# Kernel tuning notes

Measured on AMD Instinct MI355X. Metric: run time of the kernel, lower is better.

Reference implementation:

```python
import jax, jax.numpy as jnp
import numpy as np

B, S, C, H = 2, 2048, 1024, 16
D = C // H  # head dim = 64


def setup_inputs() -> dict:
    key = jax.random.key(0)
    ks = jax.random.split(key, 11)
    scale = 1.0 / np.sqrt(C)
    inp = {
        "q": jax.random.normal(ks[0], (B, S, C), dtype=jnp.float32),
        "k": jax.random.normal(ks[1], (B, S, C), dtype=jnp.float32),
        "v": jax.random.normal(ks[2], (B, S, C), dtype=jnp.float32),
        "wq": jax.random.normal(ks[3], (C, C), dtype=jnp.float32) * scale,
        "bq": jnp.zeros((C,), dtype=jnp.float32),
        "wk": jax.random.normal(ks[4], (C, C), dtype=jnp.float32) * scale,
        "bk": jnp.zeros((C,), dtype=jnp.float32),
        "wv": jax.random.normal(ks[5], (C, C), dtype=jnp.float32) * scale,
        "bv": jnp.zeros((C,), dtype=jnp.float32),
        "wo": jax.random.normal(ks[6], (C, C), dtype=jnp.float32) * scale,
        "bo": jnp.zeros((C,), dtype=jnp.float32),
    }
    return inp


def _split_heads(x):
    # [B,S,C] -> [B,H,S,D]
    b, s, _ = x.shape
    return x.reshape(b, s, H, D).transpose(0, 2, 1, 3)


def reference(q, k, v, wq, bq, wk, bk, wv, bv, wo, bo):
    qh = _split_heads(q @ wq + bq)
    kh = _split_heads(k @ wk + bk)
    vh = _split_heads(v @ wv + bv)
    scale = 1.0 / jnp.sqrt(jnp.asarray(D, dtype=qh.dtype))
    scores = jnp.einsum("bhqd,bhkd->bhqk", qh, kh) * scale  # [B,H,S,S]
    attn = jax.nn.softmax(scores, axis=-1)
    out = jnp.einsum("bhqk,bhkd->bhqd", attn, vh)  # [B,H,S,D]
    out = out.transpose(0, 2, 1, 3).reshape(q.shape[0], -1, C)  # [B,S,C]
    out = out @ wo + bo
    return out, attn
```

## Files before the change

kernel.cpp:

```cpp
#include <hip/hip_runtime.h>


#define S_  2048
#define C_  1024
#define H_  16
#define D_  64
#define BS_ 4096
#define BH_ 32

typedef unsigned short ushort_t;
typedef __attribute__((ext_vector_type(8))) short short8;
typedef __attribute__((ext_vector_type(4))) float floatx4;

#define GLDS16(gp, lp) __builtin_amdgcn_global_load_lds( \
    (__attribute__((address_space(1))) void*)(gp), \
    (__attribute__((address_space(3))) void*)(lp), 16, 0, 0)

#define MFMA16(a, b, c) __builtin_amdgcn_mfma_f32_16x16x32_bf16((a), (b), (c), 0, 0, 0)

__device__ __forceinline__ ushort_t f2bf(float x) {
  union { float f; unsigned u; } v; v.f = x;
  unsigned r = v.u + 0x7fffu + ((v.u >> 16) & 1u);
  return (ushort_t)(r >> 16);
}
__device__ __forceinline__ float bf2f(ushort_t h) {
  union { unsigned u; float f; } v; v.u = ((unsigned)h) << 16; return v.f;
}

__global__ __launch_bounds__(256) void split_plain(
    const float* __restrict__ in, ushort_t* __restrict__ hi, ushort_t* __restrict__ lo)
{
  const int i = blockIdx.x * 256 + threadIdx.x;
  float4 v = ((const float4*)in)[i];
  ushort4 h, l;
  h.x = f2bf(v.x); l.x = f2bf(v.x - bf2f(h.x));
  h.y = f2bf(v.y); l.y = f2bf(v.y - bf2f(h.y));
  h.z = f2bf(v.z); l.z = f2bf(v.z - bf2f(h.z));
  h.w = f2bf(v.w); l.w = f2bf(v.w - bf2f(h.w));
  ((ushort4*)hi)[i] = h;
  ((ushort4*)lo)[i] = l;
}

__global__ __launch_bounds__(256) void split_T(
    const float* __restrict__ W, ushort_t* __restrict__ THi, ushort_t* __restrict__ TLo)
{
  __shared__ float t[64][65];
  const int k0 = blockIdx.x * 64, n0 = blockIdx.y * 64;
  const int tid = threadIdx.x;
  const int r = tid >> 4, c4 = (tid & 15) * 4;
#pragma unroll
  for (int p = 0; p < 4; ++p) {
    float4 v = *(const float4*)&W[(size_t)(k0 + p * 16 + r) * C_ + n0 + c4];
    t[p * 16 + r][c4 + 0] = v.x;
    t[p * 16 + r][c4 + 1] = v.y;
    t[p * 16 + r][c4 + 2] = v.z;
    t[p * 16 + r][c4 + 3] = v.w;
  }
  __syncthreads();
  const int n = tid >> 2, kc = (tid & 3) * 16;
#pragma unroll
  for (int j = 0; j < 16; ++j) {
    float x = t[kc + j][n];
    ushort_t h = f2bf(x);
    const size_t idx = (size_t)(n0 + n) * C_ + k0 + kc + j;
    THi[idx] = h;
    TLo[idx] = f2bf(x - bf2f(h));
  }
}

__global__ __launch_bounds__(256) void gemm_proj(
    const ushort_t* __restrict__ Ahi, const ushort_t* __restrict__ Alo,
    const ushort_t* __restrict__ Bhi, const ushort_t* __restrict__ Blo,
    const float* __restrict__ bias,
    ushort_t* __restrict__ OHi, ushort_t* __restrict__ OLo,
    float* __restrict__ OF, int mode)
{
  __shared__ ushort_t sA[2][128 * 32];
  __shared__ ushort_t sB[2][64 * 32];

  const int tid = threadIdx.x;
  const int wv = tid >> 6, ln = tid & 63;
  const int lq = ln >> 4, lr = ln & 15;
  const int wr = wv >> 1, wc = wv & 1;
  const int r0 = blockIdx.x * 128, c0 = blockIdx.y * 64;

  const int sar = wv * 32 + (ln >> 2);
  const int sbr = wv * 16 + (ln >> 2);
  const int skc = (ln & 3) * 8;

  floatx4 acc[4][2];
#pragma unroll
  for (int m = 0; m < 4; ++m)
#pragma unroll
    for (int n = 0; n < 2; ++n) acc[m][n] = (floatx4){0.f, 0.f, 0.f, 0.f};

  for (int kt = 0; kt < 1024; kt += 32) {
    __syncthreads();
#pragma unroll
    for (int c = 0; c < 2; ++c) {
      const int row = sar + c * 16;
      GLDS16(&Ahi[(size_t)(r0 + row) * 1024 + kt + skc], &sA[0][(wv * 32 + c * 16) * 32]);
      GLDS16(&Alo[(size_t)(r0 + row) * 1024 + kt + skc], &sA[1][(wv * 32 + c * 16) * 32]);
    }
    GLDS16(&Bhi[(size_t)(c0 + sbr) * 1024 + kt + skc], &sB[0][(wv * 16) * 32]);
    GLDS16(&Blo[(size_t)(c0 + sbr) * 1024 + kt + skc], &sB[1][(wv * 16) * 32]);
    __syncthreads();

    short8 af[4][2], bf[2][2];
#pragma unroll
    for (int t = 0; t < 4; ++t) {
      af[t][0] = *(const short8*)&sA[0][(wr * 64 + t * 16 + lr) * 32 + lq * 8];
      af[t][1] = *(const short8*)&sA[1][(wr * 64 + t * 16 + lr) * 32 + lq * 8];
    }
#pragma unroll
    for (int t = 0; t < 2; ++t) {
      bf[t][0] = *(const short8*)&sB[0][(wc * 32 + t * 16 + lr) * 32 + lq * 8];
      bf[t][1] = *(const short8*)&sB[1][(wc * 32 + t * 16 + lr) * 32 + lq * 8];
    }
#pragma unroll
    for (int m = 0; m < 4; ++m)
#pragma unroll
      for (int n = 0; n < 2; ++n) {
        acc[m][n] = MFMA16(af[m][1], bf[n][0], acc[m][n]);
        acc[m][n] = MFMA16(af[m][0], bf[n][1], acc[m][n]);
        acc[m][n] = MFMA16(af[m][0], bf[n][0], acc[m][n]);
      }
  }

#pragma unroll
  for (int m = 0; m < 4; ++m) {
    const int grb = r0 + wr * 64 + m * 16 + lq * 4;
#pragma unroll
    for (int n = 0; n < 2; ++n) {
      const int gc = c0 + wc * 32 + n * 16 + lr;
      const float bs = bias[gc];
      if (mode == 2) {
#pragma unroll
        for (int r = 0; r < 4; ++r)
          OF[(size_t)(grb + r) * C_ + gc] = acc[m][n][r] + bs;
      } else if (mode == 0) {
        const int h = gc >> 6, d = gc & 63;
#pragma unroll
        for (int r = 0; r < 4; ++r) {
          const int gr = grb + r;
          const int b = gr >> 11, s = gr & (S_ - 1);
          const size_t idx = ((size_t)(b * H_ + h) * S_ + s) * D_ + d;
          float x = acc[m][n][r] + bs;
          ushort_t hx = f2bf(x);
          OHi[idx] = hx;
          OLo[idx] = f2bf(x - bf2f(hx));
        }
      } else {
        const int h = gc >> 6, d = gc & 63;
        const int b = grb >> 11, s = grb & (S_ - 1);
        const size_t idx = ((size_t)(b * H_ + h) * D_ + d) * S_ + s;
        ushort4 hv, lv;
        float x0 = acc[m][n][0] + bs, x1 = acc[m][n][1] + bs;
        float x2 = acc[m][n][2] + bs, x3 = acc[m][n][3] + bs;
        hv.x = f2bf(x0); lv.x = f2bf(x0 - bf2f(hv.x));
        hv.y = f2bf(x1); lv.y = f2bf(x1 - bf2f(hv.y));
        hv.z = f2bf(x2); lv.z = f2bf(x2 - bf2f(hv.z));
        hv.w = f2bf(x3); lv.w = f2bf(x3 - bf2f(hv.w));
        *(ushort4*)&OHi[idx] = hv;
        *(ushort4*)&OLo[idx] = lv;
      }
    }
  }
}

__global__ __launch_bounds__(256) void scores_exp(
    const ushort_t* __restrict__ QHi, const ushort_t* __restrict__ QLo,
    const ushort_t* __restrict__ KHi, const ushort_t* __restrict__ KLo,
    float* __restrict__ E, float* __restrict__ rowsum)
{
  __shared__ ushort_t sA[2][128 * 32];
  __shared__ ushort_t sB[2][128 * 32];

  const int tid = threadIdx.x;
  const int wv = tid >> 6, ln = tid & 63;
  const int lq = ln >> 4, lr = ln & 15;
  const int wr = wv >> 1, wc = wv & 1;
  const int bh = blockIdx.z;
  const int i0 = blockIdx.x * 128, j0 = blockIdx.y * 128;

  const ushort_t* Qh = QHi + (size_t)bh * S_ * D_;
  const ushort_t* Ql = QLo + (size_t)bh * S_ * D_;
  const ushort_t* Kh = KHi + (size_t)bh * S_ * D_;
  const ushort_t* Kl = KLo + (size_t)bh * S_ * D_;

  const int sar = wv * 32 + (ln >> 2);
  const int skc = (ln & 3) * 8;

  floatx4 acc[4][4];
#pragma unroll
  for (int m = 0; m < 4; ++m)
#pragma unroll
    for (int n = 0; n < 4; ++n) acc[m][n] = (floatx4){0.f, 0.f, 0.f, 0.f};

#pragma unroll
  for (int kt = 0; kt < 64; kt += 32) {
    __syncthreads();
#pragma unroll
    for (int c = 0; c < 2; ++c) {
      const int row = sar + c * 16;
      GLDS16(&Qh[(size_t)(i0 + row) * D_ + kt + skc], &sA[0][(wv * 32 + c * 16) * 32]);
      GLDS16(&Ql[(size_t)(i0 + row) * D_ + kt + skc], &sA[1][(wv * 32 + c * 16) * 32]);
      GLDS16(&Kh[(size_t)(j0 + row) * D_ + kt + skc], &sB[0][(wv * 32 + c * 16) * 32]);
      GLDS16(&Kl[(size_t)(j0 + row) * D_ + kt + skc], &sB[1][(wv * 32 + c * 16) * 32]);
    }
    __syncthreads();

    short8 af[4][2], bf[4][2];
#pragma unroll
    for (int t = 0; t < 4; ++t) {
      af[t][0] = *(const short8*)&sA[0][(wr * 64 + t * 16 + lr) * 32 + lq * 8];
      af[t][1] = *(const short8*)&sA[1][(wr * 64 + t * 16 + lr) * 32 + lq * 8];
      bf[t][0] = *(const short8*)&sB[0][(wc * 64 + t * 16 + lr) * 32 + lq * 8];
      bf[t][1] = *(const short8*)&sB[1][(wc * 64 + t * 16 + lr) * 32 + lq * 8];
    }
#pragma unroll
    for (int m = 0; m < 4; ++m)
#pragma unroll
      for (int n = 0; n < 4; ++n) {
        acc[m][n] = MFMA16(af[m][1], bf[n][0], acc[m][n]);
        acc[m][n] = MFMA16(af[m][0], bf[n][1], acc[m][n]);
        acc[m][n] = MFMA16(af[m][0], bf[n][0], acc[m][n]);
      }
  }

  float* Eb = E + (size_t)bh * S_ * S_;
  const float cexp = 0.18033688011112042f;
#pragma unroll
  for (int m = 0; m < 4; ++m) {
    const int grb = i0 + wr * 64 + m * 16 + lq * 4;
    float ps[4] = {0.f, 0.f, 0.f, 0.f};
#pragma unroll
    for (int n = 0; n < 4; ++n) {
      const int gc = j0 + wc * 64 + n * 16 + lr;
#pragma unroll
      for (int r = 0; r < 4; ++r) {
        float e = exp2f(acc[m][n][r] * cexp);
        Eb[(size_t)(grb + r) * S_ + gc] = e;
        ps[r] += e;
      }
    }
#pragma unroll
    for (int r = 0; r < 4; ++r) {
      float s = ps[r];
      s += __shfl_xor(s, 1);
      s += __shfl_xor(s, 2);
      s += __shfl_xor(s, 4);
      s += __shfl_xor(s, 8);
      if (lr == 0) atomicAdd(&rowsum[bh * S_ + grb + r], s);
    }
  }
}

__global__ __launch_bounds__(256) void pv_attn(
    float* __restrict__ E,
    const ushort_t* __restrict__ VHi, const ushort_t* __restrict__ VLo,
    const float* __restrict__ rowsum,
    ushort_t* __restrict__ OHi, ushort_t* __restrict__ OLo)
{
  __shared__ ushort_t sA[2][128 * 32];
  __shared__ ushort_t sB[2][64 * 32];

  const int tid = threadIdx.x;
  const int wv = tid >> 6, ln = tid & 63;
  const int lq = ln >> 4, lr = ln & 15;
  const int bh = blockIdx.z, b = bh >> 4, h = bh & (H_ - 1);
  const int i0 = blockIdx.x * 128;

  float* Eb = E + (size_t)bh * S_ * S_;
  const ushort_t* Vh = VHi + (size_t)bh * D_ * S_;
  const ushort_t* Vl = VLo + (size_t)bh * D_ * S_;

  const int ar = tid >> 3;
  const int ac = (tid & 7) * 4;
  float rinv_s[4];
#pragma unroll
  for (int u = 0; u < 4; ++u)
    rinv_s[u] = 1.0f / rowsum[bh * S_ + i0 + u * 32 + ar];

  const int sbr = wv * 16 + (ln >> 2);
  const int skc = (ln & 3) * 8;

  floatx4 acc[2][4];
#pragma unroll
  for (int m = 0; m < 2; ++m)
#pragma unroll
    for (int n = 0; n < 4; ++n) acc[m][n] = (floatx4){0.f, 0.f, 0.f, 0.f};

  for (int kt = 0; kt < S_; kt += 32) {
    __syncthreads();
    GLDS16(&Vh[(size_t)sbr * S_ + kt + skc], &sB[0][(wv * 16) * 32]);
    GLDS16(&Vl[(size_t)sbr * S_ + kt + skc], &sB[1][(wv * 16) * 32]);
#pragma unroll
    for (int u = 0; u < 4; ++u) {
      const int row = u * 32 + ar;
      float4 ev = *(const float4*)&Eb[(size_t)(i0 + row) * S_ + kt + ac];
      float4 nv;
      nv.x = ev.x * rinv_s[u]; nv.y = ev.y * rinv_s[u];
      nv.z = ev.z * rinv_s[u]; nv.w = ev.w * rinv_s[u];
      *(float4*)&Eb[(size_t)(i0 + row) * S_ + kt + ac] = nv;
      ushort4 h4, l4;
      h4.x = f2bf(ev.x); l4.x = f2bf(ev.x - bf2f(h4.x));
      h4.y = f2bf(ev.y); l4.y = f2bf(ev.y - bf2f(h4.y));
      h4.z = f2bf(ev.z); l4.z = f2bf(ev.z - bf2f(h4.z));
      h4.w = f2bf(ev.w); l4.w = f2bf(ev.w - bf2f(h4.w));
      *(ushort4*)&sA[0][row * 32 + ac] = h4;
      *(ushort4*)&sA[1][row * 32 + ac] = l4;
    }
    __syncthreads();

    short8 af[2][2], bf[4][2];
#pragma unroll
    for (int t = 0; t < 2; ++t) {
      af[t][0] = *(const short8*)&sA[0][(wv * 32 + t * 16 + lr) * 32 + lq * 8];
      af[t][1] = *(const short8*)&sA[1][(wv * 32 + t * 16 + lr) * 32 + lq * 8];
    }
#pragma unroll
    for (int t = 0; t < 4; ++t) {
      bf[t][0] = *(const short8*)&sB[0][(t * 16 + lr) * 32 + lq * 8];
      bf[t][1] = *(const short8*)&sB[1][(t * 16 + lr) * 32 + lq * 8];
    }
#pragma unroll
    for (int m = 0; m < 2; ++m)
#pragma unroll
      for (int n = 0; n < 4; ++n) {
        acc[m][n] = MFMA16(af[m][1], bf[n][0], acc[m][n]);
        acc[m][n] = MFMA16(af[m][0], bf[n][1], acc[m][n]);
        acc[m][n] = MFMA16(af[m][0], bf[n][0], acc[m][n]);
      }
  }

#pragma unroll
  for (int m = 0; m < 2; ++m) {
    const int rowb = wv * 32 + m * 16 + lq * 4;
#pragma unroll
    for (int r = 0; r < 4; ++r) {
      const float rv = 1.0f / rowsum[bh * S_ + i0 + rowb + r];
      const size_t orow = (size_t)(b * S_ + i0 + rowb + r) * C_ + h * D_;
#pragma unroll
      for (int n = 0; n < 4; ++n) {
        float x = acc[m][n][r] * rv;
        ushort_t hx = f2bf(x);
        OHi[orow + n * 16 + lr] = hx;
        OLo[orow + n * 16 + lr] = f2bf(x - bf2f(hx));
      }
    }
  }
}

extern "C" void kernel_launch(void* const* d_in, const int* in_sizes, int n_in,
                              void* d_out, int out_size, void* d_ws, size_t ws_size,
                              hipStream_t stream)
{
  (void)in_sizes; (void)n_in; (void)out_size; (void)ws_size;

  const float* q  = (const float*)d_in[0];
  const float* k  = (const float*)d_in[1];
  const float* v  = (const float*)d_in[2];
  const float* wq = (const float*)d_in[3];
  const float* bq = (const float*)d_in[4];
  const float* wk = (const float*)d_in[5];
  const float* bk = (const float*)d_in[6];
  const float* wv = (const float*)d_in[7];
  const float* bv = (const float*)d_in[8];
  const float* wo = (const float*)d_in[9];
  const float* bo = (const float*)d_in[10];

  const size_t NE = (size_t)BS_ * C_;

  float* outF = (float*)d_out;
  float* Ebuf = outF + NE;
  ushort_t* XSHi = (ushort_t*)d_out;
  ushort_t* XSLo = XSHi + NE;

  ushort_t* ws16 = (ushort_t*)d_ws;
  ushort_t* QhHi = ws16;           ushort_t* QhLo = QhHi + NE;
  ushort_t* KhHi = QhLo + NE;      ushort_t* KhLo = KhHi + NE;
  ushort_t* VtHi = KhLo + NE;      ushort_t* VtLo = VtHi + NE;
  ushort_t* WtHi = VtLo + NE;      ushort_t* WtLo = WtHi + (size_t)C_ * C_;
  float* rowsum = (float*)(WtLo + (size_t)C_ * C_);

  const dim3 gS(NE / 4 / 256);
  const dim3 gT(16, 16);
  const dim3 gP(BS_ / 128, C_ / 64);
  const dim3 gSc(S_ / 128, S_ / 128, BH_);
  const dim3 gPv(S_ / 128, 1, BH_);

  split_T<<<gT, 256, 0, stream>>>(wq, WtHi, WtLo);
  split_plain<<<gS, 256, 0, stream>>>(q, XSHi, XSLo);
  gemm_proj<<<gP, 256, 0, stream>>>(XSHi, XSLo, WtHi, WtLo, bq, QhHi, QhLo, nullptr, 0);
  split_T<<<gT, 256, 0, stream>>>(wk, WtHi, WtLo);
  split_plain<<<gS, 256, 0, stream>>>(k, XSHi, XSLo);
  gemm_proj<<<gP, 256, 0, stream>>>(XSHi, XSLo, WtHi, WtLo, bk, KhHi, KhLo, nullptr, 0);
  split_T<<<gT, 256, 0, stream>>>(wv, WtHi, WtLo);
  split_plain<<<gS, 256, 0, stream>>>(v, XSHi, XSLo);
  gemm_proj<<<gP, 256, 0, stream>>>(XSHi, XSLo, WtHi, WtLo, bv, VtHi, VtLo, nullptr, 1);

  hipMemsetAsync(rowsum, 0, (size_t)BH_ * S_ * sizeof(float), stream);
  scores_exp<<<gSc, 256, 0, stream>>>(QhHi, QhLo, KhHi, KhLo, Ebuf, rowsum);

  pv_attn<<<gPv, 256, 0, stream>>>(Ebuf, VtHi, VtLo, rowsum, QhHi, QhLo);

  split_T<<<gT, 256, 0, stream>>>(wo, WtHi, WtLo);
  gemm_proj<<<gP, 256, 0, stream>>>(QhHi, QhLo, WtHi, WtLo, bo, nullptr, nullptr, outF, 2);
}
```

Baseline: 1.191 ms.

## Fuse attention into flash-style PV kernel and recompute normalized probabilities for output

```diff
diff --git a/kernel.cpp b/kernel.cpp
--- a/kernel.cpp
+++ b/kernel.cpp
@@ -168,20 +168,209 @@
   }
 }
 
-__global__ __launch_bounds__(256) void scores_exp(
+__global__ __launch_bounds__(256) void attn_pv(
     const ushort_t* __restrict__ QHi, const ushort_t* __restrict__ QLo,
     const ushort_t* __restrict__ KHi, const ushort_t* __restrict__ KLo,
-    float* __restrict__ E, float* __restrict__ rowsum)
-{
-  __shared__ ushort_t sA[2][128 * 32];
-  __shared__ ushort_t sB[2][128 * 32];
+    const ushort_t* __restrict__ VHi, const ushort_t* __restrict__ VLo,
+    float* __restrict__ rowsum,
+    ushort_t* __restrict__ OHi, ushort_t* __restrict__ OLo)
+{
+  __shared__ ushort_t sQE[2][2][128 * 32];
+  __shared__ ushort_t sK[2][2][64 * 32];
+  __shared__ ushort_t sV[2][2][64 * 32];
 
   const int tid = threadIdx.x;
   const int wv = tid >> 6, ln = tid & 63;
   const int lq = ln >> 4, lr = ln & 15;
   const int wr = wv >> 1, wc = wv & 1;
-  const int bh = blockIdx.z;
-  const int i0 = blockIdx.x * 128, j0 = blockIdx.y * 128;
+
+  const int wgid = blockIdx.x;
+  const int sw = (wgid & 7) * 64 + (wgid >> 3);
+  const int bh = sw >> 4;
+  const int i0 = (sw & 15) * 128;
+  const int b = bh >> 4, h = bh & (H_ - 1);
+
+  const ushort_t* Qh = QHi + (size_t)bh * S_ * D_;
+  const ushort_t* Ql = QLo + (size_t)bh * S_ * D_;
+  const ushort_t* Kh = KHi + (size_t)bh * S_ * D_;
+  const ushort_t* Kl = KLo + (size_t)bh * S_ * D_;
+  const ushort_t* Vh = VHi + (size_t)bh * D_ * S_;
+  const ushort_t* Vl = VLo + (size_t)bh * D_ * S_;
+
+  const int srow = ln >> 2;
+  const int skc = (ln & 3) * 8;
+
+#pragma unroll
+  for (int pl = 0; pl < 2; ++pl) {
+    const ushort_t* src = pl ? Ql : Qh;
+#pragma unroll
+    for (int kp = 0; kp < 2; ++kp)
+#pragma unroll
+      for (int c = 0; c < 2; ++c)
+        GLDS16(&src[(size_t)(i0 + wv * 32 + c * 16 + srow) * D_ + kp * 32 + skc],
+               &sQE[pl][kp][(wv * 32 + c * 16) * 32]);
+  }
+  __syncthreads();
+  short8 aq[4][2][2];
+#pragma unroll
+  for (int m = 0; m < 4; ++m)
+#pragma unroll
+    for (int kp = 0; kp < 2; ++kp)
+#pragma unroll
+      for (int pl = 0; pl < 2; ++pl)
+        aq[m][kp][pl] = *(const short8*)&sQE[pl][kp][(wr * 64 + m * 16 + lr) * 32 + lq * 8];
+
+  const float cexp = 0.18033688011112042f;
+  floatx4 acc_o[4][2];
+  float ps[4][4];
+#pragma unroll
+  for (int m = 0; m < 4; ++m) {
+#pragma unroll
+    for (int n = 0; n < 2; ++n) acc_o[m][n] = (floatx4){0.f, 0.f, 0.f, 0.f};
+#pragma unroll
+    for (int r = 0; r < 4; ++r) ps[m][r] = 0.f;
+  }
+
+  for (int jt = 0; jt < 32; ++jt) {
+    const int j0 = jt * 64;
+    __syncthreads();
+#pragma unroll
+    for (int pl = 0; pl < 2; ++pl) {
+      const ushort_t* ks = pl ? Kl : Kh;
+      const ushort_t* vs = pl ? Vl : Vh;
+#pragma unroll
+      for (int kp = 0; kp < 2; ++kp)
+        GLDS16(&ks[(size_t)(j0 + wv * 16 + srow) * D_ + kp * 32 + skc],
+               &sK[pl][kp][(wv * 16) * 32]);
+#pragma unroll
+      for (int jp = 0; jp < 2; ++jp)
+        GLDS16(&vs[(size_t)(wv * 16 + srow) * S_ + j0 + jp * 32 + skc],
+               &sV[pl][jp][(wv * 16) * 32]);
+    }
+    __syncthreads();
+
+    floatx4 acc_s[4][2];
+#pragma unroll
+    for (int m = 0; m < 4; ++m)
+#pragma unroll
+      for (int n = 0; n < 2; ++n) acc_s[m][n] = (floatx4){0.f, 0.f, 0.f, 0.f};
+#pragma unroll
+    for (int kp = 0; kp < 2; ++kp) {
+      short8 bk[2][2];
+#pragma unroll
+      for (int n = 0; n < 2; ++n)
+#pragma unroll
+        for (int pl = 0; pl < 2; ++pl)
+          bk[n][pl] = *(const short8*)&sK[pl][kp][(wc * 32 + n * 16 + lr) * 32 + lq * 8];
+#pragma unroll
+      for (int m = 0; m < 4; ++m)
+#pragma unroll
+        for (int n = 0; n < 2; ++n) {
+          acc_s[m][n] = MFMA16(aq[m][kp][1], bk[n][0], acc_s[m][n]);
+          acc_s[m][n] = MFMA16(aq[m][kp][0], bk[n][1], acc_s[m][n]);
+          acc_s[m][n] = MFMA16(aq[m][kp][0], bk[n][0], acc_s[m][n]);
+        }
+    }
+
+#pragma unroll
+    for (int m = 0; m < 4; ++m)
+#pragma unroll
+      for (int n = 0; n < 2; ++n)
+#pragma unroll
+        for (int r = 0; r < 4; ++r) {
+          float e = exp2f(acc_s[m][n][r] * cexp);
+          ps[m][r] += e;
+          ushort_t eh = f2bf(e);
+          ushort_t el = f2bf(e - bf2f(eh));
+          const int row = wr * 64 + m * 16 + lq * 4 + r;
+          sQE[0][wc][row * 32 + n * 16 + lr] = eh;
+          sQE[1][wc][row * 32 + n * 16 + lr] = el;
+        }
+    __syncthreads();
+
+#pragma unroll
+    for (int kp = 0; kp < 2; ++kp) {
+      short8 ae[4][2], bv[2][2];
+#pragma unroll
+      for (int m = 0; m < 4; ++m)
+#pragma unroll
+        for (int pl = 0; pl < 2; ++pl)
+          ae[m][pl] = *(const short8*)&sQE[pl][kp][(wr * 64 + m * 16 + lr) * 32 + lq * 8];
+#pragma unroll
+      for (int n = 0; n < 2; ++n)
+#pragma unroll
+        for (int pl = 0; pl < 2; ++pl)
+          bv[n][pl] = *(const short8*)&sV[pl][kp][(wc * 32 + n * 16 + lr) * 32 + lq * 8];
+#pragma unroll
+      for (int m = 0; m < 4; ++m)
+#pragma unroll
+        for (int n = 0; n < 2; ++n) {
+          acc_o[m][n] = MFMA16(ae[m][1], bv[n][0], acc_o[m][n]);
+          acc_o[m][n] = MFMA16(ae[m][0], bv[n][1], acc_o[m][n]);
+          acc_o[m][n] = MFMA16(ae[m][0], bv[n][0], acc_o[m][n]);
+        }
+    }
+  }
+
+  __syncthreads();
+  float* sRsp = (float*)&sV[0][0][0];
+  float* sTot = sRsp + 256;
+#pragma unroll
+  for (int m = 0; m < 4; ++m)
+#pragma unroll
+    for (int r = 0; r < 4; ++r) {
+      float s = ps[m][r];
+      s += __shfl_xor(s, 1);
+      s += __shfl_xor(s, 2);
+      s += __shfl_xor(s, 4);
+      s += __shfl_xor(s, 8);
+      if (lr == 0) sRsp[wc * 128 + wr * 64 + m * 16 + lq * 4 + r] = s;
+    }
+  __syncthreads();
+  if (tid < 128) {
+    float t = sRsp[tid] + sRsp[128 + tid];
+    sTot[tid] = t;
+    rowsum[bh * S_ + i0 + tid] = t;
+  }
+  __syncthreads();
+
+#pragma unroll
+  for (int m = 0; m < 4; ++m) {
+    const int rows = wr * 64 + m * 16 + lq * 4;
+#pragma unroll
+    for (int r = 0; r < 4; ++r) {
+      const float rv = 1.0f / sTot[rows + r];
+      const size_t orow = (size_t)(b * S_ + i0 + rows + r) * C_ + h * D_;
+#pragma unroll
+      for (int n = 0; n < 2; ++n) {
+        const int d = wc * 32 + n * 16 + lr;
+        float x = acc_o[m][n][r] * rv;
+        ushort_t hx = f2bf(x);
+        OHi[orow + d] = hx;
+        OLo[orow + d] = f2bf(x - bf2f(hx));
+      }
+    }
+  }
+}
+
+__global__ __launch_bounds__(256) void attn_write(
+    const ushort_t* __restrict__ QHi, const ushort_t* __restrict__ QLo,
+    const ushort_t* __restrict__ KHi, const ushort_t* __restrict__ KLo,
+    const float* __restrict__ rowsum, float* __restrict__ attn)
+{
+  __shared__ ushort_t sA[2][128 * 32];
+  __shared__ ushort_t sB[2][128 * 32];
+
+  const int tid = threadIdx.x;
+  const int wv = tid >> 6, ln = tid & 63;
+  const int lq = ln >> 4, lr = ln & 15;
+  const int wr = wv >> 1, wc = wv & 1;
+
+  const int wgid = blockIdx.x;
+  const int sw = (wgid & 7) * 1024 + (wgid >> 3);
+  const int bh = sw >> 8;
+  const int t8 = sw & 255;
+  const int i0 = (t8 >> 4) * 128, j0 = (t8 & 15) * 128;
 
   const ushort_t* Qh = QHi + (size_t)bh * S_ * D_;
   const ushort_t* Ql = QLo + (size_t)bh * S_ * D_;
@@ -228,128 +417,31 @@
       }
   }
 
-  float* Eb = E + (size_t)bh * S_ * S_;
+  float* Eb = attn + (size_t)bh * S_ * S_;
   const float cexp = 0.18033688011112042f;
 #pragma unroll
   for (int m = 0; m < 4; ++m) {
     const int grb = i0 + wr * 64 + m * 16 + lq * 4;
-    float ps[4] = {0.f, 0.f, 0.f, 0.f};
+    float rv[4];
+#pragma unroll
+    for (int r = 0; r < 4; ++r) rv[r] = 1.0f / rowsum[bh * S_ + grb + r];
 #pragma unroll
     for (int n = 0; n < 4; ++n) {
       const int gc = j0 + wc * 64 + n * 16 + lr;
 #pragma unroll
       for (int r = 0; r < 4; ++r) {
-        float e = exp2f(acc[m][n][r] * cexp);
-        Eb[(size_t)(grb + r) * S_ + gc] = e;
-        ps[r] += e;
+        float e = exp2f(acc[m][n][r] * cexp) * rv[r];
+        __builtin_nontemporal_store(e, &Eb[(size_t)(grb + r) * S_ + gc]);
       }
     }
-#pragma unroll
-    for (int r = 0; r < 4; ++r) {
-      float s = ps[r];
-      s += __shfl_xor(s, 1);
-      s += __shfl_xor(s, 2);
-      s += __shfl_xor(s, 4);
-      s += __shfl_xor(s, 8);
-      if (lr == 0) atomicAdd(&rowsum[bh * S_ + grb + r], s);
-    }
-  }
-}
-
-__global__ __launch_bounds__(256) void pv_attn(
-    float* __restrict__ E,
-    const ushort_t* __restrict__ VHi, const ushort_t* __restrict__ VLo,
-    const float* __restrict__ rowsum,
-    ushort_t* __restrict__ OHi, ushort_t* __restrict__ OLo)
-{
-  __shared__ ushort_t sA[2][128 * 32];
-  __shared__ ushort_t sB[2][64 * 32];
-
-  const int tid = threadIdx.x;
-  const int wv = tid >> 6, ln = tid & 63;
-  const int lq = ln >> 4, lr = ln & 15;
-  const int bh = blockIdx.z, b = bh >> 4, h = bh & (H_ - 1);
-  const int i0 = blockIdx.x * 128;
-
-  float* Eb = E + (size_t)bh * S_ * S_;
-  const ushort_t* Vh = VHi + (size_t)bh * D_ * S_;
-  const ushort_t* Vl = VLo + (size_t)bh * D_ * S_;
-
-  const int ar = tid >> 3;
-  const int ac = (tid & 7) * 4;
-  float rinv_s[4];
-#pragma unroll
-  for (int u = 0; u < 4; ++u)
-    rinv_s[u] = 1.0f / rowsum[bh * S_ + i0 + u * 32 + ar];
-
-  const int sbr = wv * 16 + (ln >> 2);
-  const int skc = (ln & 3) * 8;
-
-  floatx4 acc[2][4];
-#pragma unroll
-  for (int m = 0; m < 2; ++m)
-#pragma unroll
-    for (int n = 0; n < 4; ++n) acc[m][n] = (floatx4){0.f, 0.f, 0.f, 0.f};
-
-  for (int kt = 0; kt < S_; kt += 32) {
-    __syncthreads();
-    GLDS16(&Vh[(size_t)sbr * S_ + kt + skc], &sB[0][(wv * 16) * 32]);
-    GLDS16(&Vl[(size_t)sbr * S_ + kt + skc], &sB[1][(wv * 16) * 32]);
-#pragma unroll
-    for (int u = 0; u < 4; ++u) {
-      const int row = u * 32 + ar;
-      float4 ev = *(const float4*)&Eb[(size_t)(i0 + row) * S_ + kt + ac];
-      float4 nv;
-      nv.x = ev.x * rinv_s[u]; nv.y = ev.y * rinv_s[u];
-      nv.z = ev.z * rinv_s[u]; nv.w = ev.w * rinv_s[u];
-      *(float4*)&Eb[(size_t)(i0 + row) * S_ + kt + ac] = nv;
-      ushort4 h4, l4;
-      h4.x = f2bf(ev.x); l4.x = f2bf(ev.x - bf2f(h4.x));
-      h4.y = f2bf(ev.y); l4.y = f2bf(ev.y - bf2f(h4.y));
-      h4.z = f2bf(ev.z); l4.z = f2bf(ev.z - bf2f(h4.z));
-      h4.w = f2bf(ev.w); l4.w = f2bf(ev.w - bf2f(h4.w));
-      *(ushort4*)&sA[0][row * 32 + ac] = h4;
-      *(ushort4*)&sA[1][row * 32 + ac] = l4;
-    }
-    __syncthreads();
-
-    short8 af[2][2], bf[4][2];
-#pragma unroll
-    for (int t = 0; t < 2; ++t) {
-      af[t][0] = *(const short8*)&sA[0][(wv * 32 + t * 16 + lr) * 32 + lq * 8];
-      af[t][1] = *(const short8*)&sA[1][(wv * 32 + t * 16 + lr) * 32 + lq * 8];
-    }
-#pragma unroll
-    for (int t = 0; t < 4; ++t) {
-      bf[t][0] = *(const short8*)&sB[0][(t * 16 + lr) * 32 + lq * 8];
-      bf[t][1] = *(const short8*)&sB[1][(t * 16 + lr) * 32 + lq * 8];
-    }
-#pragma unroll
-    for (int m = 0; m < 2; ++m)
-#pragma unroll
-      for (int n = 0; n < 4; ++n) {
-        acc[m][n] = MFMA16(af[m][1], bf[n][0], acc[m][n]);
-        acc[m][n] = MFMA16(af[m][0], bf[n][1], acc[m][n]);
-        acc[m][n] = MFMA16(af[m][0], bf[n][0], acc[m][n]);
-      }
-  }
-
-#pragma unroll
-  for (int m = 0; m < 2; ++m) {
-    const int rowb = wv * 32 + m * 16 + lq * 4;
-#pragma unroll
-    for (int r = 0; r < 4; ++r) {
-      const float rv = 1.0f / rowsum[bh * S_ + i0 + rowb + r];
-      const size_t orow = (size_t)(b * S_ + i0 + rowb + r) * C_ + h * D_;
-#pragma unroll
-      for (int n = 0; n < 4; ++n) {
-        float x = acc[m][n][r] * rv;
-        ushort_t hx = f2bf(x);
-        OHi[orow + n * 16 + lr] = hx;
-        OLo[orow + n * 16 + lr] = f2bf(x - bf2f(hx));
-      }
-    }
-  }
+  }
+}
+
+__global__ __launch_bounds__(256) void copy4(
+    const float* __restrict__ in, float* __restrict__ out)
+{
+  const int i = blockIdx.x * 256 + threadIdx.x;
+  ((float4*)out)[i] = ((const float4*)in)[i];
 }
 
 extern "C" void kernel_launch(void* const* d_in, const int* in_sizes, int n_in,
@@ -387,8 +479,6 @@
   const dim3 gS(NE / 4 / 256);
   const dim3 gT(16, 16);
   const dim3 gP(BS_ / 128, C_ / 64);
-  const dim3 gSc(S_ / 128, S_ / 128, BH_);
-  const dim3 gPv(S_ / 128, 1, BH_);
 
   split_T<<<gT, 256, 0, stream>>>(wq, WtHi, WtLo);
   split_plain<<<gS, 256, 0, stream>>>(q, XSHi, XSLo);
@@ -400,11 +490,12 @@
   split_plain<<<gS, 256, 0, stream>>>(v, XSHi, XSLo);
   gemm_proj<<<gP, 256, 0, stream>>>(XSHi, XSLo, WtHi, WtLo, bv, VtHi, VtLo, nullptr, 1);
 
-  hipMemsetAsync(rowsum, 0, (size_t)BH_ * S_ * sizeof(float), stream);
-  scores_exp<<<gSc, 256, 0, stream>>>(QhHi, QhLo, KhHi, KhLo, Ebuf, rowsum);
-
-  pv_attn<<<gPv, 256, 0, stream>>>(Ebuf, VtHi, VtLo, rowsum, QhHi, QhLo);
+  attn_pv<<<dim3(512), 256, 0, stream>>>(QhHi, QhLo, KhHi, KhLo, VtHi, VtLo,
+                                         rowsum, XSHi, XSLo);
+  attn_write<<<dim3(8192), 256, 0, stream>>>(QhHi, QhLo, KhHi, KhLo, rowsum, Ebuf);
 
   split_T<<<gT, 256, 0, stream>>>(wo, WtHi, WtLo);
-  gemm_proj<<<gP, 256, 0, stream>>>(QhHi, QhLo, WtHi, WtLo, bo, nullptr, nullptr, outF, 2);
-}
+  float* tmpF = (float*)QhHi;
+  gemm_proj<<<gP, 256, 0, stream>>>(XSHi, XSLo, WtHi, WtLo, bo, nullptr, nullptr, tmpF, 2);
+  copy4<<<dim3(NE / 4 / 256), 256, 0, stream>>>(tmpF, outF);
+}
```

Result: faster. 967.1 us (-18.8%).
